# Performance work log

Measured on AMD Instinct MI355X. Metric: run time of the kernel, lower is better.

Reference implementation:

```python
import jax, jax.numpy as jnp
import numpy as np

E, T, H, I, K = 8, 8192, 1024, 4096, 2  # experts, tokens, hidden, intermediate, top_k


def setup_inputs() -> dict:
    key = jax.random.key(0)
    k1, k2, k3, k4 = jax.random.split(key, 4)
    return {
        "hidden_states": jax.random.normal(k1, (T, H), dtype=jnp.float32),
        "router_weight": jax.random.normal(k2, (E, H), dtype=jnp.float32) * 0.02,
        "gate_up_proj": jax.random.normal(k3, (E, 2 * I, H), dtype=jnp.float32) * 0.02,
        "down_proj": jax.random.normal(k4, (E, H, I), dtype=jnp.float32) * 0.02,
    }


def reference(hidden_states, router_weight, gate_up_proj, down_proj):
    x = hidden_states  # [T, H]
    # --- TopKRouter ---
    router_logits = x @ router_weight.T  # [T, E]
    routing_probs = jax.nn.softmax(router_logits.astype(jnp.float32), axis=-1)
    top_k_weights, top_k_indices = jax.lax.top_k(routing_probs, K)  # [T, K]
    top_k_weights = top_k_weights / jnp.sum(top_k_weights, axis=-1, keepdims=True)  # norm_topk_prob
    top_k_weights = top_k_weights.astype(router_logits.dtype)
    # --- MoEExperts: dense combine weight per (token, expert) ---
    # w_dense[t, e] = sum_k top_k_weights[t, k] * (top_k_indices[t, k] == e)
    tok = jnp.arange(x.shape[0])[:, None]
    w_dense = jnp.zeros((x.shape[0], E), dtype=x.dtype).at[tok, top_k_indices].add(top_k_weights)
    out = jnp.zeros_like(x)
    for e in range(E):  # fixed small expert loop (structurally distinct weights)
        gu = x @ gate_up_proj[e].T          # [T, 2I]
        gate, up = jnp.split(gu, 2, axis=-1)
        y = (jax.nn.silu(gate) * up) @ down_proj[e].T  # [T, H]
        out = out + w_dense[:, e:e + 1] * y
    return out
```

## Files before the change

### kernel.cpp

```cpp
#include <hip/hip_runtime.h>
#include <stdint.h>
#include <math.h>

#define NE 8
#define NT 8192
#define NH 1024
#define NI 4096
#define BM 128
#define BK 32

typedef _Float16 half8 __attribute__((ext_vector_type(8)));
typedef float f32x4 __attribute__((ext_vector_type(4)));

#define OFF_X16   (512u << 10)
#define OFF_ACT   (18u << 20)
#define OFF_GUP16 (146ull << 20)
#define OFF_DP16  (274ull << 20)

__device__ __forceinline__ half8 pack_half8(float4 a, float4 b) {
  half8 h;
  h[0] = (_Float16)a.x; h[1] = (_Float16)a.y; h[2] = (_Float16)a.z; h[3] = (_Float16)a.w;
  h[4] = (_Float16)b.x; h[5] = (_Float16)b.y; h[6] = (_Float16)b.z; h[7] = (_Float16)b.w;
  return h;
}

__device__ __forceinline__ void gload16(const void* g, void* l) {
  __builtin_amdgcn_global_load_lds(
      (const __attribute__((address_space(1))) uint32_t*)g,
      (__attribute__((address_space(3))) uint32_t*)l, 16, 0, 0);
}

#define PIPE_WAIT(N) asm volatile("s_waitcnt vmcnt(" #N ")" ::: "memory")
#define PIPE_BAR() do { asm volatile("" ::: "memory"); \
                        __builtin_amdgcn_s_barrier(); \
                        asm volatile("" ::: "memory"); } while (0)

__global__ __launch_bounds__(256) void convert_w(
    const float* __restrict__ src, _Float16* __restrict__ dst, int n8)
{
  int stride = gridDim.x * 256;
  for (int i = blockIdx.x * 256 + threadIdx.x; i < n8; i += stride) {
    const float4* p = (const float4*)(src + (size_t)i * 8);
    float4 a = p[0], b = p[1];
    *(half8*)(dst + (size_t)i * 8) = pack_half8(a, b);
  }
}

__global__ __launch_bounds__(256) void moe_router(
    const float* __restrict__ x, const float* __restrict__ rw,
    int* __restrict__ iws, _Float16* __restrict__ x16)
{
  int wid  = threadIdx.x >> 6;
  int lane = threadIdx.x & 63;
  int t = (blockIdx.x << 2) + wid;

  const float4* xp4 = (const float4*)(x + (size_t)t * NH + lane * 16);
  float xv[16];
  #pragma unroll
  for (int j = 0; j < 4; ++j) {
    float4 v = xp4[j];
    xv[4*j+0] = v.x; xv[4*j+1] = v.y; xv[4*j+2] = v.z; xv[4*j+3] = v.w;
  }
  half8 h0, h1;
  #pragma unroll
  for (int j = 0; j < 8; ++j) { h0[j] = (_Float16)xv[j]; h1[j] = (_Float16)xv[8+j]; }
  half8* xo = (half8*)(x16 + (size_t)t * NH + lane * 16);
  xo[0] = h0; xo[1] = h1;

  float lg[NE];
  #pragma unroll
  for (int e = 0; e < NE; ++e) {
    const float4* wp4 = (const float4*)(rw + e * NH + lane * 16);
    float s = 0.f;
    #pragma unroll
    for (int j = 0; j < 4; ++j) {
      float4 w = wp4[j];
      s += xv[4*j+0]*w.x + xv[4*j+1]*w.y + xv[4*j+2]*w.z + xv[4*j+3]*w.w;
    }
    lg[e] = s;
  }
  #pragma unroll
  for (int d = 32; d > 0; d >>= 1) {
    #pragma unroll
    for (int e = 0; e < NE; ++e) lg[e] += __shfl_xor(lg[e], d, 64);
  }
  if (lane == 0) {
    int e0 = 0;
    #pragma unroll
    for (int e = 1; e < NE; ++e) if (lg[e] > lg[e0]) e0 = e;
    int e1 = (e0 == 0) ? 1 : 0;
    #pragma unroll
    for (int e = 0; e < NE; ++e) if (e != e0 && lg[e] > lg[e1]) e1 = e;
    float p1 = expf(lg[e1] - lg[e0]);
    float s  = 1.f + p1;
    int*   te = iws + 64;
    float* tw = (float*)(iws + 64 + NT*2);
    te[2*t]   = e0; te[2*t+1] = e1;
    tw[2*t]   = 1.f / s; tw[2*t+1] = p1 / s;
    atomicAdd(iws + e0, 1);
    atomicAdd(iws + e1, 1);
  }
}

__global__ void moe_scan(int* iws) {
  if (threadIdx.x == 0 && blockIdx.x == 0) {
    int* cnt = iws; int* off = iws + 8; int* mbc = iws + 25;
    int o = 0, m = 0;
    for (int e = 0; e < NE; ++e) {
      off[e] = o; mbc[e] = m;
      o += cnt[e]; m += (cnt[e] + BM - 1) / BM;
    }
    off[NE] = o; mbc[NE] = m;
  }
}

__global__ __launch_bounds__(256) void moe_fill(int* __restrict__ iws) {
  int t = blockIdx.x * 256 + threadIdx.x;
  const int*   te = iws + 64;
  const float* tw = (const float*)(iws + 64 + NT*2);
  int*   cursor   = iws + 17;
  const int* off  = iws + 8;
  int*   tok_slot = iws + 64 + NT*4;
  float* w_slot   = (float*)(iws + 64 + NT*6);
  #pragma unroll
  for (int k = 0; k < 2; ++k) {
    int e = te[2*t+k];
    int pos = atomicAdd(&cursor[e], 1);
    int s = off[e] + pos;
    tok_slot[s] = t;
    w_slot[s]   = tw[2*t+k];
  }
}


__global__ __launch_bounds__(256, 2) void moe_gemm1_f16(
    const _Float16* __restrict__ x16, const _Float16* __restrict__ gup16,
    const int* __restrict__ iws, _Float16* __restrict__ act)
{
  const int* cnt = iws; const int* off = iws + 8; const int* mbc = iws + 25;
  const int* tok_slot = iws + 64 + NT*4;
  int bid = blockIdx.x;
  int mb  = bid >> 6;
  int i0  = (bid & 63) << 6;
  if (mb >= mbc[NE]) return;
  int e = 0;
  while (mb >= mbc[e+1]) ++e;
  int mloc  = mb - mbc[e];
  int row0  = off[e] + mloc * BM;
  int nrows = cnt[e] - mloc * BM; if (nrows > BM) nrows = BM;

  __shared__ __align__(16) _Float16 Al [3][BM * BK];
  __shared__ __align__(16) _Float16 Bgl[3][64 * BK];
  __shared__ __align__(16) _Float16 Bul[3][64 * BK];

  int tid = threadIdx.x, wid = tid >> 6, lane = tid & 63;
  int sr0 = wid*16 + (lane >> 2);
  int sr1 = 64 + sr0;
  int slot = lane & 3;
  int ks0 = (slot ^ ((sr0 >> 1) & 3)) * 8;
  int ks1 = (slot ^ ((sr1 >> 1) & 3)) * 8;

  int tok0 = tok_slot[row0 + (sr0 < nrows ? sr0 : 0)];
  int tok1 = tok_slot[row0 + (sr1 < nrows ? sr1 : 0)];
  const _Float16* pA0 = x16 + (size_t)tok0 * NH + ks0;
  const _Float16* pA1 = x16 + (size_t)tok1 * NH + ks1;
  const _Float16* pBg = gup16 + ((size_t)e*2*NI + i0 + sr0) * NH + ks0;
  const _Float16* pBu = pBg + (size_t)NI * NH;

  int wr = (wid >> 1) * 64, wc = (wid & 1) * 32;
  int fr = lane & 15, fq = lane >> 4;

  f32x4 accG[4][2] = {};
  f32x4 accU[4][2] = {};

  _Float16 *A0 = &Al[0][0], *A1 = &Al[1][0], *A2 = &Al[2][0];
  _Float16 *G0 = &Bgl[0][0], *G1 = &Bgl[1][0], *G2 = &Bgl[2][0];
  _Float16 *U0 = &Bul[0][0], *U1 = &Bul[1][0], *U2 = &Bul[2][0];

#define STAGE1(Ab, Gb, Ub, kk) do { \
    gload16(pA0 + (kk), (Ab) + wid*512); \
    gload16(pA1 + (kk), (Ab) + (4+wid)*512); \
    gload16(pBg + (kk), (Gb) + wid*512); \
    gload16(pBu + (kk), (Ub) + wid*512); \
  } while (0)

#define COMPUTE1(Ab, Gb, Ub) do { \
    half8 aF[4]; \
    _Pragma("unroll") \
    for (int m = 0; m < 4; ++m) { \
      int r = wr + m*16 + fr; \
      aF[m] = *(const half8*)((Ab) + r*BK + ((fq ^ ((r>>1)&3)) * 8)); \
    } \
    __builtin_amdgcn_s_setprio(1); \
    _Pragma("unroll") \
    for (int n = 0; n < 2; ++n) { \
      int rb = wc + n*16 + fr; \
      int bo = rb*BK + ((fq ^ ((rb>>1)&3)) * 8); \
      half8 bg = *(const half8*)((Gb) + bo); \
      half8 bu = *(const half8*)((Ub) + bo); \
      _Pragma("unroll") \
      for (int m = 0; m < 4; ++m) \
        accG[m][n] = __builtin_amdgcn_mfma_f32_16x16x32_f16(aF[m], bg, accG[m][n], 0, 0, 0); \
      _Pragma("unroll") \
      for (int m = 0; m < 4; ++m) \
        accU[m][n] = __builtin_amdgcn_mfma_f32_16x16x32_f16(aF[m], bu, accU[m][n], 0, 0, 0); \
    } \
    __builtin_amdgcn_s_setprio(0); \
  } while (0)

#define ROT1() do { _Float16* t_; \
    t_ = A0; A0 = A1; A1 = A2; A2 = t_; \
    t_ = G0; G0 = G1; G1 = G2; G2 = t_; \
    t_ = U0; U0 = U1; U1 = U2; U2 = t_; } while (0)

  STAGE1(A0, G0, U0, 0);
  STAGE1(A1, G1, U1, BK);

  for (int k0 = 0; k0 + 2*BK < NH; k0 += BK) {
    PIPE_WAIT(4);
    PIPE_BAR();
    STAGE1(A2, G2, U2, k0 + 2*BK);
    COMPUTE1(A0, G0, U0);
    ROT1();
  }
  PIPE_WAIT(4);
  PIPE_BAR();
  COMPUTE1(A0, G0, U0);
  ROT1();
  PIPE_WAIT(0);
  PIPE_BAR();
  COMPUTE1(A0, G0, U0);

#undef STAGE1
#undef COMPUTE1
#undef ROT1

  #pragma unroll
  for (int m = 0; m < 4; ++m) {
    #pragma unroll
    for (int j = 0; j < 4; ++j) {
      int rl = wr + m*16 + fq*4 + j;
      if (rl < nrows) {
        _Float16* dst = act + (size_t)(row0 + rl) * NI + i0 + wc + fr;
        #pragma unroll
        for (int n = 0; n < 2; ++n) {
          float g = accG[m][n][j], u = accU[m][n][j];
          float a = (g / (1.f + __expf(-g))) * u;
          dst[n*16] = (_Float16)a;
        }
      }
    }
  }
}

__global__ __launch_bounds__(256, 2) void moe_gemm2_f16(
    const _Float16* __restrict__ act, const _Float16* __restrict__ dp16,
    const int* __restrict__ iws, float* __restrict__ out)
{
  const int* cnt = iws; const int* off = iws + 8; const int* mbc = iws + 25;
  const int* tok_slot = iws + 64 + NT*4;
  const float* w_slot = (const float*)(iws + 64 + NT*6);
  int bid = blockIdx.x;
  int mb  = bid >> 3;
  int h0  = (bid & 7) << 7;
  if (mb >= mbc[NE]) return;
  int e = 0;
  while (mb >= mbc[e+1]) ++e;
  int mloc  = mb - mbc[e];
  int row0  = off[e] + mloc * BM;
  int nrows = cnt[e] - mloc * BM; if (nrows > BM) nrows = BM;

  __shared__ __align__(16) _Float16 Al[3][BM  * BK];
  __shared__ __align__(16) _Float16 Bl[3][128 * BK];

  int tid = threadIdx.x, wid = tid >> 6, lane = tid & 63;
  int sr0 = wid*16 + (lane >> 2);
  int sr1 = 64 + sr0;
  int slot = lane & 3;
  int ks0 = (slot ^ ((sr0 >> 1) & 3)) * 8;
  int ks1 = (slot ^ ((sr1 >> 1) & 3)) * 8;

  const _Float16* pA0 = act + (size_t)(row0 + (sr0 < nrows ? sr0 : 0)) * NI + ks0;
  const _Float16* pA1 = act + (size_t)(row0 + (sr1 < nrows ? sr1 : 0)) * NI + ks1;
  const _Float16* pB0 = dp16 + ((size_t)e*NH + h0 + sr0) * NI + ks0;
  const _Float16* pB1 = dp16 + ((size_t)e*NH + h0 + sr1) * NI + ks1;

  int wr = (wid >> 1) * 64, wc = (wid & 1) * 64;
  int fr = lane & 15, fq = lane >> 4;

  f32x4 acc[4][4] = {};

  _Float16 *A0 = &Al[0][0], *A1 = &Al[1][0], *A2 = &Al[2][0];
  _Float16 *B0 = &Bl[0][0], *B1 = &Bl[1][0], *B2 = &Bl[2][0];

#define STAGE2(Ab, Bb, kk) do { \
    gload16(pA0 + (kk), (Ab) + wid*512); \
    gload16(pA1 + (kk), (Ab) + (4+wid)*512); \
    gload16(pB0 + (kk), (Bb) + wid*512); \
    gload16(pB1 + (kk), (Bb) + (4+wid)*512); \
  } while (0)

#define COMPUTE2(Ab, Bb) do { \
    half8 aF[4]; \
    _Pragma("unroll") \
    for (int m = 0; m < 4; ++m) { \
      int r = wr + m*16 + fr; \
      aF[m] = *(const half8*)((Ab) + r*BK + ((fq ^ ((r>>1)&3)) * 8)); \
    } \
    __builtin_amdgcn_s_setprio(1); \
    _Pragma("unroll") \
    for (int n = 0; n < 4; ++n) { \
      int rb = wc + n*16 + fr; \
      half8 b = *(const half8*)((Bb) + rb*BK + ((fq ^ ((rb>>1)&3)) * 8)); \
      _Pragma("unroll") \
      for (int m = 0; m < 4; ++m) \
        acc[m][n] = __builtin_amdgcn_mfma_f32_16x16x32_f16(aF[m], b, acc[m][n], 0, 0, 0); \
    } \
    __builtin_amdgcn_s_setprio(0); \
  } while (0)

#define ROT2() do { _Float16* t_; \
    t_ = A0; A0 = A1; A1 = A2; A2 = t_; \
    t_ = B0; B0 = B1; B1 = B2; B2 = t_; } while (0)

  STAGE2(A0, B0, 0);
  STAGE2(A1, B1, BK);

  for (int k0 = 0; k0 + 2*BK < NI; k0 += BK) {
    PIPE_WAIT(4);
    PIPE_BAR();
    STAGE2(A2, B2, k0 + 2*BK);
    COMPUTE2(A0, B0);
    ROT2();
  }
  PIPE_WAIT(4);
  PIPE_BAR();
  COMPUTE2(A0, B0);
  ROT2();
  PIPE_WAIT(0);
  PIPE_BAR();
  COMPUTE2(A0, B0);

#undef STAGE2
#undef COMPUTE2
#undef ROT2

  #pragma unroll
  for (int m = 0; m < 4; ++m) {
    #pragma unroll
    for (int j = 0; j < 4; ++j) {
      int rl = wr + m*16 + fq*4 + j;
      if (rl < nrows) {
        int slotr = row0 + rl;
        float wgt = w_slot[slotr];
        int tok   = tok_slot[slotr];
        float* dst = out + (size_t)tok * NH + h0 + wc + fr;
        #pragma unroll
        for (int n = 0; n < 4; ++n)
          atomicAdd(dst + n*16, acc[m][n][j] * wgt);
      }
    }
  }
}

extern "C" void kernel_launch(void* const* d_in, const int* in_sizes, int n_in,
                              void* d_out, int out_size, void* d_ws, size_t ws_size,
                              hipStream_t stream) {
  const float* x   = (const float*)d_in[0];
  const float* rw  = (const float*)d_in[1];
  const float* gup = (const float*)d_in[2];
  const float* dp  = (const float*)d_in[3];
  float* out = (float*)d_out;
  int* iws = (int*)d_ws;
  _Float16* x16   = (_Float16*)((char*)d_ws + OFF_X16);
  _Float16* act   = (_Float16*)((char*)d_ws + OFF_ACT);
  _Float16* gup16 = (_Float16*)((char*)d_ws + OFF_GUP16);
  _Float16* dp16  = (_Float16*)((char*)d_ws + OFF_DP16);

  hipMemsetAsync(d_out, 0, (size_t)NT * NH * sizeof(float), stream);
  hipMemsetAsync(d_ws, 0, 512, stream);

  convert_w<<<4096, 256, 0, stream>>>(gup, gup16, NE*2*NI*NH/8);
  convert_w<<<4096, 256, 0, stream>>>(dp,  dp16,  NE*NH*NI/8);

  moe_router<<<NT / 4, 256, 0, stream>>>(x, rw, iws, x16);
  moe_scan<<<1, 64, 0, stream>>>(iws);
  moe_fill<<<NT / 256, 256, 0, stream>>>(iws);

  int nmb = NT * 2 / BM + NE;
  moe_gemm1_f16<<<nmb * (NI / 64), 256, 0, stream>>>(x16, gup16, iws, act);
  moe_gemm2_f16<<<nmb * (NH / 128), 256, 0, stream>>>(act, dp16, iws, out);
}
```

Baseline: 984.1 us.

## Enlarge down-projection GEMM tile to 256x256 with 512 threads and interleaved staging

Reworks the second expert GEMM to use 256-row by 256-column tiles computed by 8 waves of 512 threads. It adds a separate per-expert block count for 256-row blocks, and splits the next-stage global loads so they are issued between the two halves of the MFMA work. The larger tile is meant to raise arithmetic intensity and cut redundant weight and activation loads. The costs are higher register and LDS pressure, a single block per CU, and more padding waste on the last partial row block of each expert.

Result: slower. 1.004 ms (+2.0%).

```diff
diff --git a/kernel.cpp b/kernel.cpp
--- a/kernel.cpp
+++ b/kernel.cpp
@@ -104,13 +104,15 @@
 
 __global__ void moe_scan(int* iws) {
   if (threadIdx.x == 0 && blockIdx.x == 0) {
-    int* cnt = iws; int* off = iws + 8; int* mbc = iws + 25;
-    int o = 0, m = 0;
+    int* cnt = iws; int* off = iws + 8; int* mbc = iws + 25; int* mbc2 = iws + 34;
+    int o = 0, m = 0, m2 = 0;
     for (int e = 0; e < NE; ++e) {
-      off[e] = o; mbc[e] = m;
-      o += cnt[e]; m += (cnt[e] + BM - 1) / BM;
+      off[e] = o; mbc[e] = m; mbc2[e] = m2;
+      o += cnt[e];
+      m  += (cnt[e] + BM - 1) / BM;
+      m2 += (cnt[e] + 255) / 256;
     }
-    off[NE] = o; mbc[NE] = m;
+    off[NE] = o; mbc[NE] = m; mbc2[NE] = m2;
   }
 }
 
@@ -131,7 +133,6 @@
     w_slot[s]   = tw[2*t+k];
   }
 }
-
 
 __global__ __launch_bounds__(256, 2) void moe_gemm1_f16(
     const _Float16* __restrict__ x16, const _Float16* __restrict__ gup16,
@@ -253,69 +254,83 @@
   }
 }
 
-__global__ __launch_bounds__(256, 2) void moe_gemm2_f16(
+__global__ __launch_bounds__(512, 1) void moe_gemm2_f16(
     const _Float16* __restrict__ act, const _Float16* __restrict__ dp16,
     const int* __restrict__ iws, float* __restrict__ out)
 {
-  const int* cnt = iws; const int* off = iws + 8; const int* mbc = iws + 25;
+  const int* cnt = iws; const int* off = iws + 8; const int* mbc2 = iws + 34;
   const int* tok_slot = iws + 64 + NT*4;
   const float* w_slot = (const float*)(iws + 64 + NT*6);
   int bid = blockIdx.x;
-  int mb  = bid >> 3;
-  int h0  = (bid & 7) << 7;
-  if (mb >= mbc[NE]) return;
+  int mb  = bid >> 2;
+  int h0  = (bid & 3) << 8;
+  if (mb >= mbc2[NE]) return;
   int e = 0;
-  while (mb >= mbc[e+1]) ++e;
-  int mloc  = mb - mbc[e];
-  int row0  = off[e] + mloc * BM;
-  int nrows = cnt[e] - mloc * BM; if (nrows > BM) nrows = BM;
-
-  __shared__ __align__(16) _Float16 Al[3][BM  * BK];
-  __shared__ __align__(16) _Float16 Bl[3][128 * BK];
+  while (mb >= mbc2[e+1]) ++e;
+  int mloc  = mb - mbc2[e];
+  int row0  = off[e] + mloc * 256;
+  int nrows = cnt[e] - mloc * 256; if (nrows > 256) nrows = 256;
+
+  __shared__ __align__(16) _Float16 As[3][256 * BK];
+  __shared__ __align__(16) _Float16 Bs[3][256 * BK];
 
   int tid = threadIdx.x, wid = tid >> 6, lane = tid & 63;
-  int sr0 = wid*16 + (lane >> 2);
-  int sr1 = 64 + sr0;
-  int slot = lane & 3;
-  int ks0 = (slot ^ ((sr0 >> 1) & 3)) * 8;
-  int ks1 = (slot ^ ((sr1 >> 1) & 3)) * 8;
-
-  const _Float16* pA0 = act + (size_t)(row0 + (sr0 < nrows ? sr0 : 0)) * NI + ks0;
-  const _Float16* pA1 = act + (size_t)(row0 + (sr1 < nrows ? sr1 : 0)) * NI + ks1;
-  const _Float16* pB0 = dp16 + ((size_t)e*NH + h0 + sr0) * NI + ks0;
-  const _Float16* pB1 = dp16 + ((size_t)e*NH + h0 + sr1) * NI + ks1;
-
-  int wr = (wid >> 1) * 64, wc = (wid & 1) * 64;
+  int srow = tid >> 2;
+  int slot = tid & 3;
+  int ks   = (slot ^ ((srow >> 1) & 3)) * 8;
+
+  int ar0 = row0 + srow;       if (ar0 > NT*2 - 1) ar0 = NT*2 - 1;
+  int ar1 = row0 + 128 + srow; if (ar1 > NT*2 - 1) ar1 = NT*2 - 1;
+  const _Float16* pA0 = act + (size_t)ar0 * NI + ks;
+  const _Float16* pA1 = act + (size_t)ar1 * NI + ks;
+  const _Float16* pB0 = dp16 + ((size_t)e*NH + h0 + srow) * NI + ks;
+  const _Float16* pB1 = pB0 + (size_t)128 * NI;
+
+  int wr = (wid >> 2) * 128, wc = (wid & 3) * 64;
   int fr = lane & 15, fq = lane >> 4;
 
-  f32x4 acc[4][4] = {};
-
-  _Float16 *A0 = &Al[0][0], *A1 = &Al[1][0], *A2 = &Al[2][0];
-  _Float16 *B0 = &Bl[0][0], *B1 = &Bl[1][0], *B2 = &Bl[2][0];
-
-#define STAGE2(Ab, Bb, kk) do { \
-    gload16(pA0 + (kk), (Ab) + wid*512); \
-    gload16(pA1 + (kk), (Ab) + (4+wid)*512); \
-    gload16(pB0 + (kk), (Bb) + wid*512); \
-    gload16(pB1 + (kk), (Bb) + (4+wid)*512); \
+  f32x4 acc[8][4] = {};
+
+  _Float16 *A0 = &As[0][0], *A1 = &As[1][0], *A2 = &As[2][0];
+  _Float16 *B0 = &Bs[0][0], *B1 = &Bs[1][0], *B2 = &Bs[2][0];
+
+#define STG2(Ab, Bb, kk) do { \
+    gload16(pA0 + (kk), (Ab) + tid*8); \
+    gload16(pA1 + (kk), (Ab) + 4096 + tid*8); \
+    gload16(pB0 + (kk), (Bb) + tid*8); \
+    gload16(pB1 + (kk), (Bb) + 4096 + tid*8); \
   } while (0)
 
-#define COMPUTE2(Ab, Bb) do { \
-    half8 aF[4]; \
-    _Pragma("unroll") \
-    for (int m = 0; m < 4; ++m) { \
-      int r = wr + m*16 + fr; \
-      aF[m] = *(const half8*)((Ab) + r*BK + ((fq ^ ((r>>1)&3)) * 8)); \
+#define LDF(B,r) (*(const half8*)((B) + (size_t)(r)*BK + ((fq ^ (((r)>>1)&3)) * 8)))
+
+#define COMPUTE2(Ab, Bb, DO_STAGE, kk) do { \
+    half8 aF[8]; \
+    _Pragma("unroll") \
+    for (int m = 0; m < 8; ++m) aF[m] = LDF((Ab), wr + m*16 + fr); \
+    half8 bF[4]; \
+    _Pragma("unroll") \
+    for (int n = 0; n < 4; ++n) bF[n] = LDF((Bb), wc + n*16 + fr); \
+    if (DO_STAGE) { \
+      gload16(pA0 + (kk), A2 + tid*8); \
+      gload16(pA1 + (kk), A2 + 4096 + tid*8); \
     } \
     __builtin_amdgcn_s_setprio(1); \
     _Pragma("unroll") \
-    for (int n = 0; n < 4; ++n) { \
-      int rb = wc + n*16 + fr; \
-      half8 b = *(const half8*)((Bb) + rb*BK + ((fq ^ ((rb>>1)&3)) * 8)); \
+    for (int n = 0; n < 4; ++n) \
       _Pragma("unroll") \
       for (int m = 0; m < 4; ++m) \
-        acc[m][n] = __builtin_amdgcn_mfma_f32_16x16x32_f16(aF[m], b, acc[m][n], 0, 0, 0); \
+        acc[m][n] = __builtin_amdgcn_mfma_f32_16x16x32_f16(aF[m], bF[n], acc[m][n], 0, 0, 0); \
+    __builtin_amdgcn_s_setprio(0); \
+    if (DO_STAGE) { \
+      gload16(pB0 + (kk), B2 + tid*8); \
+      gload16(pB1 + (kk), B2 + 4096 + tid*8); \
     } \
+    __builtin_amdgcn_s_setprio(1); \
+    _Pragma("unroll") \
+    for (int n = 0; n < 4; ++n) \
+      _Pragma("unroll") \
+      for (int m = 4; m < 8; ++m) \
+        acc[m][n] = __builtin_amdgcn_mfma_f32_16x16x32_f16(aF[m], bF[n], acc[m][n], 0, 0, 0); \
     __builtin_amdgcn_s_setprio(0); \
   } while (0)
 
@@ -323,30 +338,30 @@
     t_ = A0; A0 = A1; A1 = A2; A2 = t_; \
     t_ = B0; B0 = B1; B1 = B2; B2 = t_; } while (0)
 
-  STAGE2(A0, B0, 0);
-  STAGE2(A1, B1, BK);
+  STG2(A0, B0, 0);
+  STG2(A1, B1, BK);
 
   for (int k0 = 0; k0 + 2*BK < NI; k0 += BK) {
     PIPE_WAIT(4);
     PIPE_BAR();
-    STAGE2(A2, B2, k0 + 2*BK);
-    COMPUTE2(A0, B0);
+    COMPUTE2(A0, B0, 1, k0 + 2*BK);
     ROT2();
   }
   PIPE_WAIT(4);
   PIPE_BAR();
-  COMPUTE2(A0, B0);
+  COMPUTE2(A0, B0, 0, 0);
   ROT2();
   PIPE_WAIT(0);
   PIPE_BAR();
-  COMPUTE2(A0, B0);
-
-#undef STAGE2
+  COMPUTE2(A0, B0, 0, 0);
+
+#undef STG2
+#undef LDF
 #undef COMPUTE2
 #undef ROT2
 
   #pragma unroll
-  for (int m = 0; m < 4; ++m) {
+  for (int m = 0; m < 8; ++m) {
     #pragma unroll
     for (int j = 0; j < 4; ++j) {
       int rl = wr + m*16 + fq*4 + j;
@@ -389,5 +404,5 @@
 
   int nmb = NT * 2 / BM + NE;
   moe_gemm1_f16<<<nmb * (NI / 64), 256, 0, stream>>>(x16, gup16, iws, act);
-  moe_gemm2_f16<<<nmb * (NH / 128), 256, 0, stream>>>(act, dp16, iws, out);
-}
+  moe_gemm2_f16<<<72 * 4, 512, 0, stream>>>(act, dp16, iws, out);
+}
```
